# Kernel optimization log

Measured on AMD Instinct MI355X. Metric: run time of the kernel, lower is better.

## Reference

```python
import jax, jax.numpy as jnp
import numpy as np

NUM_HEADS = 8

def setup_inputs() -> dict:
    key = jax.random.key(0)
    kq, kk, kv = jax.random.split(key, 3)
    shape = (8, 12, 512, 256)  # (batch, in_steps, num_nodes, model_dim)
    return {
        "query": jax.random.normal(kq, shape, dtype=jnp.float32),
        "key": jax.random.normal(kk, shape, dtype=jnp.float32),
        "value": jax.random.normal(kv, shape, dtype=jnp.float32),
    }

def reference(query, key, value):
    # torch split(dim=-1)/cat(dim=0) == reshape feature dim into (H, head_dim)
    # contiguous chunks; heads stay independent so math matches standard MHA.
    B, T, Nq, D = query.shape
    Nk = key.shape[-2]
    H = NUM_HEADS
    d = D // H
    q = query.reshape(B, T, Nq, H, d)
    k = key.reshape(B, T, Nk, H, d)
    v = value.reshape(B, T, Nk, H, d)
    # scores: (B, T, H, Nq, Nk)
    scores = jnp.einsum("btqhd,btkhd->bthqk", q, k) / jnp.sqrt(jnp.asarray(d, q.dtype))
    attn = jax.nn.softmax(scores, axis=-1)
    out = jnp.einsum("bthqk,btkhd->btqhd", attn, v)
    return out.reshape(B, T, Nq, D)
```

## Files before the change

### kernel.cpp

```cpp
#include <hip/hip_runtime.h>
#include <hip/hip_bf16.h>


#define N_    512
#define DM    256
#define DH    32
#define CHUNK 512

typedef __attribute__((ext_vector_type(8))) short bf16x8;
typedef __attribute__((ext_vector_type(4))) float f32x4;

__device__ __forceinline__ unsigned short f2bf(float f) {
    unsigned int u = __builtin_bit_cast(unsigned int, f);
    return (unsigned short)((u + 0x8000u) >> 16);
}

__device__ __forceinline__ unsigned int pack_hi16(float a, float b) {
    return __builtin_amdgcn_perm(__builtin_bit_cast(unsigned int, b),
                                 __builtin_bit_cast(unsigned int, a),
                                 0x07060302u);
}

__device__ __forceinline__ unsigned int pack_lo16(unsigned int lo, unsigned int hi) {
    return __builtin_amdgcn_perm(hi, lo, 0x05040100u);
}

__device__ __forceinline__ int fxor(int d) {
    return ((d >> 2) ^ ((d & 3) << 1)) & 7;
}

__global__ __launch_bounds__(512, 4) void attn_mha_kernel(
    const float* __restrict__ Q, const float* __restrict__ K,
    const float* __restrict__ V, float* __restrict__ O)
{
    __shared__ unsigned short kls[CHUNK * DH];
    __shared__ unsigned short vtls[DH * CHUNK];

    const int tid = threadIdx.x;
    const int bt = blockIdx.x >> 3;
    const int h  = blockIdx.x & 7;
    const size_t base = (size_t)bt * (N_ * DM) + (size_t)h * DH;
    const float* Qg = Q + base;
    const float* Kg = K + base;
    const float* Vg = V + base;
    float*       Og = O + base;

    const int wave = tid >> 6;
    const int lane = tid & 63;
    const int lr = lane & 15;
    const int lh = lane >> 4;

    const float QSC = 32.64105756f;
    const int kslot = (lh ^ ((lr >> 1) & 3)) * 8;

    bf16x8 qf[4];
    #pragma unroll
    for (int t = 0; t < 4; ++t) {
        const int q0 = wave * 64 + t * 16;
        const float* qp = Qg + (size_t)(q0 + lr) * DM + lh * 8;
        const float4 qa = *(const float4*)qp;
        const float4 qb = *(const float4*)(qp + 4);
        bf16x8 q;
        q[0] = (short)f2bf(qa.x * QSC); q[1] = (short)f2bf(qa.y * QSC);
        q[2] = (short)f2bf(qa.z * QSC); q[3] = (short)f2bf(qa.w * QSC);
        q[4] = (short)f2bf(qb.x * QSC); q[5] = (short)f2bf(qb.y * QSC);
        q[6] = (short)f2bf(qb.z * QSC); q[7] = (short)f2bf(qb.w * QSC);
        qf[t] = q;
    }

    bf16x8 ones;
    #pragma unroll
    for (int i = 0; i < 8; ++i) ones[i] = (short)0x3F80;

    f32x4 o0[4], o1[4], lsa[4];
    #pragma unroll
    for (int t = 0; t < 4; ++t) {
        o0[t]  = (f32x4){0.f, 0.f, 0.f, 0.f};
        o1[t]  = (f32x4){0.f, 0.f, 0.f, 0.f};
        lsa[t] = (f32x4){0.f, 0.f, 0.f, 0.f};
    }

    const f32x4 minit = {14714.92f, 14714.92f, 14714.92f, 14714.92f};

    {
        const int d4 = tid & 7;
        const int r0 = tid >> 3;
        #pragma unroll 2
        for (int p = 0; p < 8; ++p) {
            const int kvl = p * 64 + r0;
            const float4 kf = *(const float4*)(Kg + (size_t)kvl * DM + d4 * 4);
            const int slot = (d4 >> 1) ^ ((kvl >> 1) & 3);
            ushort4 w;
            w.x = f2bf(kf.x); w.y = f2bf(kf.y); w.z = f2bf(kf.z); w.w = f2bf(kf.w);
            *(ushort4*)(&kls[kvl * 32 + slot * 8 + (d4 & 1) * 4]) = w;
        }
        #pragma unroll 2
        for (int p = 0; p < 4; ++p) {
            const int m = p * 64 + r0;
            const int grp = m >> 4;
            const int w   = m & 15;
            const int kvl = grp * 32 + ((w & 1) << 4) + ((w >> 1) << 1);
            const float* vp = Vg + (size_t)kvl * DM + d4 * 4;
            const float4 a = *(const float4*)vp;
            const float4 b = *(const float4*)(vp + DM);
            const float av[4] = {a.x, a.y, a.z, a.w};
            const float bv[4] = {b.x, b.y, b.z, b.w};
            const int pp  = ((kvl >> 2) & 3) * 8 + ((kvl >> 4) & 1) * 4 + (kvl & 3);
            const int idx = (kvl & ~31) + pp;
            const int g  = idx >> 3;
            const int go = idx & 7;
            #pragma unroll
            for (int i = 0; i < 4; ++i) {
                const int d = d4 * 4 + i;
                const unsigned int pk = pack_hi16(av[i], bv[i]);
                *(unsigned int*)(&vtls[d * CHUNK + (g ^ fxor(d)) * 8 + go]) = pk;
            }
        }
    }
    __syncthreads();

    #pragma unroll 1
    for (int it = 0; it < 16; ++it) {
        const int c0 = it * 32;

        const bf16x8 kb0 = *(const bf16x8*)(&kls[(c0 + lr) * 32 + kslot]);
        const bf16x8 kb1 = *(const bf16x8*)(&kls[(c0 + 16 + lr) * 32 + kslot]);
        const int G = it * 4 + lh;
        const bf16x8 vb0 = *(const bf16x8*)(&vtls[lr * CHUNK + (G ^ fxor(lr)) * 8]);
        const bf16x8 vb1 = *(const bf16x8*)(&vtls[(16 + lr) * CHUNK + (G ^ fxor(16 + lr)) * 8]);

        #pragma unroll
        for (int gq = 0; gq < 2; ++gq) {
            f32x4 s0[2], s1[2];
            #pragma unroll
            for (int u = 0; u < 2; ++u) {
                const int t = gq * 2 + u;
                s0[u] = __builtin_amdgcn_mfma_f32_16x16x32_bf16(kb0, qf[t], minit, 0, 0, 0);
                s1[u] = __builtin_amdgcn_mfma_f32_16x16x32_bf16(kb1, qf[t], minit, 0, 0, 0);
            }
            #pragma unroll
            for (int u = 0; u < 2; ++u) {
                const int t = gq * 2 + u;
                unsigned int e00 = (unsigned int)(int)s0[u][0];
                unsigned int e01 = (unsigned int)(int)s0[u][1];
                unsigned int e02 = (unsigned int)(int)s0[u][2];
                unsigned int e03 = (unsigned int)(int)s0[u][3];
                unsigned int e10 = (unsigned int)(int)s1[u][0];
                unsigned int e11 = (unsigned int)(int)s1[u][1];
                unsigned int e12 = (unsigned int)(int)s1[u][2];
                unsigned int e13 = (unsigned int)(int)s1[u][3];

                union { unsigned int w[4]; bf16x8 v; } pa;
                pa.w[0] = pack_lo16(e00, e01);
                pa.w[1] = pack_lo16(e02, e03);
                pa.w[2] = pack_lo16(e10, e11);
                pa.w[3] = pack_lo16(e12, e13);

                lsa[t] = __builtin_amdgcn_mfma_f32_16x16x32_bf16(pa.v, ones, lsa[t], 0, 0, 0);
                o0[t]  = __builtin_amdgcn_mfma_f32_16x16x32_bf16(pa.v, vb0, o0[t], 0, 0, 0);
                o1[t]  = __builtin_amdgcn_mfma_f32_16x16x32_bf16(pa.v, vb1, o1[t], 0, 0, 0);
            }
        }
    }

    #pragma unroll
    for (int t = 0; t < 4; ++t) {
        #pragma unroll
        for (int r = 0; r < 4; ++r) {
            const float inv = 1.0f / lsa[t][r];
            float* orow = Og + (size_t)(wave * 64 + t * 16 + lh * 4 + r) * DM;
            orow[lr]      = o0[t][r] * inv;
            orow[16 + lr] = o1[t][r] * inv;
        }
    }
}

extern "C" void kernel_launch(void* const* d_in, const int* in_sizes, int n_in,
                              void* d_out, int out_size, void* d_ws, size_t ws_size,
                              hipStream_t stream) {
    const float* Q = (const float*)d_in[0];
    const float* K = (const float*)d_in[1];
    const float* V = (const float*)d_in[2];
    float* O = (float*)d_out;
    attn_mha_kernel<<<dim3(96 * 8), dim3(512), 0, stream>>>(Q, K, V, O);
}
```

Before: 46.38 us.

## Use persistent 1024-thread blocks processing three head slices each

Launches one 1024-thread block per CU, and each block loops over three (batch-step, head) slices. Each of the 16 waves handles 32 query rows instead of 64. This is meant to cut block scheduling overhead and spread the per-slice work across more waves. In exchange, K/V staging is serialized with compute across iterations, with an extra barrier between slices, and cross-block overlap within a CU is reduced.

```diff
diff --git a/kernel.cpp b/kernel.cpp
--- a/kernel.cpp
+++ b/kernel.cpp
@@ -29,7 +29,7 @@
     return ((d >> 2) ^ ((d & 3) << 1)) & 7;
 }
 
-__global__ __launch_bounds__(512, 4) void attn_mha_kernel(
+__global__ __launch_bounds__(1024, 4) void attn_mha_kernel(
     const float* __restrict__ Q, const float* __restrict__ K,
     const float* __restrict__ V, float* __restrict__ O)
 {
@@ -37,14 +37,6 @@
     __shared__ unsigned short vtls[DH * CHUNK];
 
     const int tid = threadIdx.x;
-    const int bt = blockIdx.x >> 3;
-    const int h  = blockIdx.x & 7;
-    const size_t base = (size_t)bt * (N_ * DM) + (size_t)h * DH;
-    const float* Qg = Q + base;
-    const float* Kg = K + base;
-    const float* Vg = V + base;
-    float*       Og = O + base;
-
     const int wave = tid >> 6;
     const int lane = tid & 63;
     const int lr = lane & 15;
@@ -53,102 +45,108 @@
     const float QSC = 32.64105756f;
     const int kslot = (lh ^ ((lr >> 1) & 3)) * 8;
 
-    bf16x8 qf[4];
-    #pragma unroll
-    for (int t = 0; t < 4; ++t) {
-        const int q0 = wave * 64 + t * 16;
-        const float* qp = Qg + (size_t)(q0 + lr) * DM + lh * 8;
-        const float4 qa = *(const float4*)qp;
-        const float4 qb = *(const float4*)(qp + 4);
-        bf16x8 q;
-        q[0] = (short)f2bf(qa.x * QSC); q[1] = (short)f2bf(qa.y * QSC);
-        q[2] = (short)f2bf(qa.z * QSC); q[3] = (short)f2bf(qa.w * QSC);
-        q[4] = (short)f2bf(qb.x * QSC); q[5] = (short)f2bf(qb.y * QSC);
-        q[6] = (short)f2bf(qb.z * QSC); q[7] = (short)f2bf(qb.w * QSC);
-        qf[t] = q;
-    }
-
     bf16x8 ones;
     #pragma unroll
     for (int i = 0; i < 8; ++i) ones[i] = (short)0x3F80;
 
-    f32x4 o0[4], o1[4], lsa[4];
-    #pragma unroll
-    for (int t = 0; t < 4; ++t) {
-        o0[t]  = (f32x4){0.f, 0.f, 0.f, 0.f};
-        o1[t]  = (f32x4){0.f, 0.f, 0.f, 0.f};
-        lsa[t] = (f32x4){0.f, 0.f, 0.f, 0.f};
-    }
-
     const f32x4 minit = {14714.92f, 14714.92f, 14714.92f, 14714.92f};
 
-    {
-        const int d4 = tid & 7;
-        const int r0 = tid >> 3;
-        #pragma unroll 2
-        for (int p = 0; p < 8; ++p) {
-            const int kvl = p * 64 + r0;
-            const float4 kf = *(const float4*)(Kg + (size_t)kvl * DM + d4 * 4);
-            const int slot = (d4 >> 1) ^ ((kvl >> 1) & 3);
-            ushort4 w;
-            w.x = f2bf(kf.x); w.y = f2bf(kf.y); w.z = f2bf(kf.z); w.w = f2bf(kf.w);
-            *(ushort4*)(&kls[kvl * 32 + slot * 8 + (d4 & 1) * 4]) = w;
+    #pragma unroll 1
+    for (int hh = 0; hh < 3; ++hh) {
+        const int f  = blockIdx.x * 3 + hh;
+        const int bt = f >> 3;
+        const int h  = f & 7;
+        const size_t base = (size_t)bt * (N_ * DM) + (size_t)h * DH;
+        const float* Qg = Q + base;
+        const float* Kg = K + base;
+        const float* Vg = V + base;
+        float*       Og = O + base;
+
+        bf16x8 qf[2];
+        #pragma unroll
+        for (int t = 0; t < 2; ++t) {
+            const int q0 = wave * 32 + t * 16;
+            const float* qp = Qg + (size_t)(q0 + lr) * DM + lh * 8;
+            const float4 qa = *(const float4*)qp;
+            const float4 qb = *(const float4*)(qp + 4);
+            bf16x8 q;
+            q[0] = (short)f2bf(qa.x * QSC); q[1] = (short)f2bf(qa.y * QSC);
+            q[2] = (short)f2bf(qa.z * QSC); q[3] = (short)f2bf(qa.w * QSC);
+            q[4] = (short)f2bf(qb.x * QSC); q[5] = (short)f2bf(qb.y * QSC);
+            q[6] = (short)f2bf(qb.z * QSC); q[7] = (short)f2bf(qb.w * QSC);
+            qf[t] = q;
         }
-        #pragma unroll 2
-        for (int p = 0; p < 4; ++p) {
-            const int m = p * 64 + r0;
-            const int grp = m >> 4;
-            const int w   = m & 15;
-            const int kvl = grp * 32 + ((w & 1) << 4) + ((w >> 1) << 1);
-            const float* vp = Vg + (size_t)kvl * DM + d4 * 4;
-            const float4 a = *(const float4*)vp;
-            const float4 b = *(const float4*)(vp + DM);
-            const float av[4] = {a.x, a.y, a.z, a.w};
-            const float bv[4] = {b.x, b.y, b.z, b.w};
-            const int pp  = ((kvl >> 2) & 3) * 8 + ((kvl >> 4) & 1) * 4 + (kvl & 3);
-            const int idx = (kvl & ~31) + pp;
-            const int g  = idx >> 3;
-            const int go = idx & 7;
-            #pragma unroll
-            for (int i = 0; i < 4; ++i) {
-                const int d = d4 * 4 + i;
-                const unsigned int pk = pack_hi16(av[i], bv[i]);
-                *(unsigned int*)(&vtls[d * CHUNK + (g ^ fxor(d)) * 8 + go]) = pk;
+
+        if (hh) __syncthreads();
+
+        {
+            const int d4 = tid & 7;
+            const int r0 = tid >> 3;
+            #pragma unroll 2
+            for (int p = 0; p < 4; ++p) {
+                const int kvl = p * 128 + r0;
+                const float4 kf = *(const float4*)(Kg + (size_t)kvl * DM + d4 * 4);
+                const int slot = (d4 >> 1) ^ ((kvl >> 1) & 3);
+                ushort4 w;
+                w.x = f2bf(kf.x); w.y = f2bf(kf.y); w.z = f2bf(kf.z); w.w = f2bf(kf.w);
+                *(ushort4*)(&kls[kvl * 32 + slot * 8 + (d4 & 1) * 4]) = w;
+            }
+            #pragma unroll 2
+            for (int p = 0; p < 2; ++p) {
+                const int m = p * 128 + r0;
+                const int grp = m >> 4;
+                const int w   = m & 15;
+                const int kvl = grp * 32 + ((w & 1) << 4) + ((w >> 1) << 1);
+                const float* vp = Vg + (size_t)kvl * DM + d4 * 4;
+                const float4 a = *(const float4*)vp;
+                const float4 b = *(const float4*)(vp + DM);
+                const float av[4] = {a.x, a.y, a.z, a.w};
+                const float bv[4] = {b.x, b.y, b.z, b.w};
+                const int pp  = ((kvl >> 2) & 3) * 8 + ((kvl >> 4) & 1) * 4 + (kvl & 3);
+                const int idx = (kvl & ~31) + pp;
+                const int g  = idx >> 3;
+                const int go = idx & 7;
+                #pragma unroll
+                for (int i = 0; i < 4; ++i) {
+                    const int d = d4 * 4 + i;
+                    const unsigned int pk = pack_hi16(av[i], bv[i]);
+                    *(unsigned int*)(&vtls[d * CHUNK + (g ^ fxor(d)) * 8 + go]) = pk;
+                }
             }
         }
-    }
-    __syncthreads();
+        __syncthreads();
 
-    #pragma unroll 1
-    for (int it = 0; it < 16; ++it) {
-        const int c0 = it * 32;
+        f32x4 o0[2], o1[2], lsa[2];
+        #pragma unroll
+        for (int t = 0; t < 2; ++t) {
+            o0[t]  = (f32x4){0.f, 0.f, 0.f, 0.f};
+            o1[t]  = (f32x4){0.f, 0.f, 0.f, 0.f};
+            lsa[t] = (f32x4){0.f, 0.f, 0.f, 0.f};
+        }
 
-        const bf16x8 kb0 = *(const bf16x8*)(&kls[(c0 + lr) * 32 + kslot]);
-        const bf16x8 kb1 = *(const bf16x8*)(&kls[(c0 + 16 + lr) * 32 + kslot]);
-        const int G = it * 4 + lh;
-        const bf16x8 vb0 = *(const bf16x8*)(&vtls[lr * CHUNK + (G ^ fxor(lr)) * 8]);
-        const bf16x8 vb1 = *(const bf16x8*)(&vtls[(16 + lr) * CHUNK + (G ^ fxor(16 + lr)) * 8]);
+        #pragma unroll 1
+        for (int it = 0; it < 16; ++it) {
+            const int c0 = it * 32;
 
-        #pragma unroll
-        for (int gq = 0; gq < 2; ++gq) {
-            f32x4 s0[2], s1[2];
+            const bf16x8 kb0 = *(const bf16x8*)(&kls[(c0 + lr) * 32 + kslot]);
+            const bf16x8 kb1 = *(const bf16x8*)(&kls[(c0 + 16 + lr) * 32 + kslot]);
+            const int G = it * 4 + lh;
+            const bf16x8 vb0 = *(const bf16x8*)(&vtls[lr * CHUNK + (G ^ fxor(lr)) * 8]);
+            const bf16x8 vb1 = *(const bf16x8*)(&vtls[(16 + lr) * CHUNK + (G ^ fxor(16 + lr)) * 8]);
+
             #pragma unroll
-            for (int u = 0; u < 2; ++u) {
-                const int t = gq * 2 + u;
-                s0[u] = __builtin_amdgcn_mfma_f32_16x16x32_bf16(kb0, qf[t], minit, 0, 0, 0);
-                s1[u] = __builtin_amdgcn_mfma_f32_16x16x32_bf16(kb1, qf[t], minit, 0, 0, 0);
-            }
-            #pragma unroll
-            for (int u = 0; u < 2; ++u) {
-                const int t = gq * 2 + u;
-                unsigned int e00 = (unsigned int)(int)s0[u][0];
-                unsigned int e01 = (unsigned int)(int)s0[u][1];
-                unsigned int e02 = (unsigned int)(int)s0[u][2];
-                unsigned int e03 = (unsigned int)(int)s0[u][3];
-                unsigned int e10 = (unsigned int)(int)s1[u][0];
-                unsigned int e11 = (unsigned int)(int)s1[u][1];
-                unsigned int e12 = (unsigned int)(int)s1[u][2];
-                unsigned int e13 = (unsigned int)(int)s1[u][3];
+            for (int t = 0; t < 2; ++t) {
+                f32x4 s0 = __builtin_amdgcn_mfma_f32_16x16x32_bf16(kb0, qf[t], minit, 0, 0, 0);
+                f32x4 s1 = __builtin_amdgcn_mfma_f32_16x16x32_bf16(kb1, qf[t], minit, 0, 0, 0);
+
+                unsigned int e00 = (unsigned int)(int)s0[0];
+                unsigned int e01 = (unsigned int)(int)s0[1];
+                unsigned int e02 = (unsigned int)(int)s0[2];
+                unsigned int e03 = (unsigned int)(int)s0[3];
+                unsigned int e10 = (unsigned int)(int)s1[0];
+                unsigned int e11 = (unsigned int)(int)s1[1];
+                unsigned int e12 = (unsigned int)(int)s1[2];
+                unsigned int e13 = (unsigned int)(int)s1[3];
 
                 union { unsigned int w[4]; bf16x8 v; } pa;
                 pa.w[0] = pack_lo16(e00, e01);
@@ -161,16 +159,16 @@
                 o1[t]  = __builtin_amdgcn_mfma_f32_16x16x32_bf16(pa.v, vb1, o1[t], 0, 0, 0);
             }
         }
-    }
 
-    #pragma unroll
-    for (int t = 0; t < 4; ++t) {
         #pragma unroll
-        for (int r = 0; r < 4; ++r) {
-            const float inv = 1.0f / lsa[t][r];
-            float* orow = Og + (size_t)(wave * 64 + t * 16 + lh * 4 + r) * DM;
-            orow[lr]      = o0[t][r] * inv;
-            orow[16 + lr] = o1[t][r] * inv;
+        for (int t = 0; t < 2; ++t) {
+            #pragma unroll
+            for (int r = 0; r < 4; ++r) {
+                const float inv = 1.0f / lsa[t][r];
+                float* orow = Og + (size_t)(wave * 32 + t * 16 + lh * 4 + r) * DM;
+                orow[lr]      = o0[t][r] * inv;
+                orow[16 + lr] = o1[t][r] * inv;
+            }
         }
     }
 }
@@ -182,5 +180,5 @@
     const float* K = (const float*)d_in[1];
     const float* V = (const float*)d_in[2];
     float* O = (float*)d_out;
-    attn_mha_kernel<<<dim3(96 * 8), dim3(512), 0, stream>>>(Q, K, V, O);
+    attn_mha_kernel<<<dim3(256), dim3(1024), 0, stream>>>(Q, K, V, O);
 }
```

Measured after the change: 52.54 us. 13.3% more time.
